# Performance work log

Hardware: AMD Instinct MI355X
Metric: run time of the kernel (lower is better)

Reference implementation:

```python
import jax, jax.numpy as jnp
import numpy as np

# Criteo-like layout
B = 16384          # batch
D = 13             # num dense features
S = 26             # num sparse fields
FEAT = 100000      # one-hot depth per sparse field
K = 64             # FM latent factor dim
TOTAL = D + S * FEAT  # width of the concatenated [dense | one-hot] vector
# column offset of each sparse field's one-hot block inside the stacked vector
OFFSETS = (D + np.arange(S) * FEAT).astype(np.int32)


def setup_inputs() -> dict:
    key = jax.random.key(0)
    k1, k2, k3, k4 = jax.random.split(key, 4)
    dense_inputs = jax.random.normal(k1, (B, D), dtype=jnp.float32)
    sparse_inputs = jax.random.randint(k2, (B, S), 0, FEAT, dtype=jnp.int32)
    # FM parameters over the full stacked feature space [dense | one-hots]
    w = jax.random.normal(k3, (TOTAL, 1), dtype=jnp.float32) * 0.01  # linear weights
    V = jax.random.normal(k4, (TOTAL, K), dtype=jnp.float32) * 0.01  # factor matrix
    b = jnp.zeros((1,), dtype=jnp.float32)                           # bias w0
    return {"dense_inputs": dense_inputs, "sparse_inputs": sparse_inputs,
            "w": w, "V": V, "b": b}


def reference(dense_inputs, sparse_inputs, w, V, b):
    # Fused gather form of: one_hot(sparse) concat dense -> FM.
    # For one-hot columns, x_i is 0/1 so x @ w == gather-sum and x @ V == gather-sum.
    idx = sparse_inputs + jnp.asarray(OFFSETS)[None, :]               # [B, S] global rows
    # ---- first-order (linear) term: x @ w + b ----
    lin = dense_inputs @ w[:D] + jnp.sum(w[idx, 0], axis=1, keepdims=True) + b  # [B, 1]
    # ---- second-order FM term: 0.5 * sum_f [ (x@V)_f^2 - (x^2 @ V^2)_f ] ----
    xv = dense_inputs @ V[:D] + jnp.sum(V[idx], axis=1)               # [B, K]
    x2v2 = (dense_inputs ** 2) @ (V[:D] ** 2) + jnp.sum(V[idx] ** 2, axis=1)  # [B, K]
    inter = 0.5 * jnp.sum(xv * xv - x2v2, axis=1, keepdims=True)      # [B, 1]
    return jax.nn.sigmoid(lin + inter)
```

## Files before the change

kernel.cpp:

```cpp
#include <hip/hip_runtime.h>
#include <math.h>

#define BATCH 16384
#define DNUM  13
#define SNUM  26
#define FEAT  100000
#define KDIM  64
#define RPW   4

__global__ __launch_bounds__(256, 4) void fm_kernel(
    const float*  __restrict__ dense,
    const int*    __restrict__ sparse,
    const float*  __restrict__ w,
    const float4* __restrict__ V4,
    const float*  __restrict__ bias,
    float*        __restrict__ out)
{
    const int wave = (blockIdx.x * blockDim.x + threadIdx.x) >> 6;
    const int lane = threadIdx.x & 63;
    const int g    = lane >> 4;
    const int t    = lane & 15;
    const int row  = wave * RPW + g;
    const int sbase = row * SNUM;

    int idx[SNUM];
    #pragma unroll
    for (int s = 0; s < SNUM; ++s)
        idx[s] = sparse[sbase + s] + DNUM + s * FEAT;

    float lin = w[sparse[sbase + t] + DNUM + t * FEAT];
    if (t < SNUM - 16)
        lin += w[sparse[sbase + t + 16] + DNUM + (t + 16) * FEAT];
    const float* drow = dense + row * DNUM;
    if (t < DNUM)
        lin += drow[t] * w[t];

    float4 xv = make_float4(0.f, 0.f, 0.f, 0.f);
    float  x2 = 0.f;
    #pragma unroll
    for (int s = 0; s < SNUM; ++s) {
        float4 v = V4[idx[s] * 16 + t];
        xv.x += v.x; xv.y += v.y; xv.z += v.z; xv.w += v.w;
        x2   += v.x * v.x + v.y * v.y + v.z * v.z + v.w * v.w;
    }

    #pragma unroll
    for (int d = 0; d < DNUM; ++d) {
        float  xd = drow[d];
        float4 v  = V4[d * 16 + t];
        xv.x += xd * v.x; xv.y += xd * v.y;
        xv.z += xd * v.z; xv.w += xd * v.w;
        x2   += xd * xd * (v.x * v.x + v.y * v.y + v.z * v.z + v.w * v.w);
    }

    float part = 0.5f * (xv.x * xv.x + xv.y * xv.y + xv.z * xv.z + xv.w * xv.w - x2)
               + lin;

    part += __shfl_xor(part, 1);
    part += __shfl_xor(part, 2);
    part += __shfl_xor(part, 4);
    part += __shfl_xor(part, 8);

    if (t == 0) {
        float z = part + bias[0];
        out[row] = 1.0f / (1.0f + expf(-z));
    }
}

extern "C" void kernel_launch(void* const* d_in, const int* in_sizes, int n_in,
                              void* d_out, int out_size, void* d_ws, size_t ws_size,
                              hipStream_t stream) {
    const float*  dense  = (const float*)d_in[0];
    const int*    sparse = (const int*)d_in[1];
    const float*  w      = (const float*)d_in[2];
    const float4* V4     = (const float4*)d_in[3];
    const float*  bias   = (const float*)d_in[4];
    float* out = (float*)d_out;

    const int rows_per_block = (256 / 64) * RPW;
    const int grid = BATCH / rows_per_block;
    fm_kernel<<<grid, 256, 0, stream>>>(dense, sparse, w, V4, bias, out);
}
```

Measured before the change: 732.2 us.

## Split each row across 32 lanes with float2 gathers in batches of seven

```diff
diff --git a/kernel.cpp b/kernel.cpp
--- a/kernel.cpp
+++ b/kernel.cpp
@@ -6,60 +6,70 @@
 #define SNUM  26
 #define FEAT  100000
 #define KDIM  64
-#define RPW   4
+#define RPW   2
+#define GB    7
 
-__global__ __launch_bounds__(256, 4) void fm_kernel(
+__global__ __launch_bounds__(256, 8) void fm_kernel(
     const float*  __restrict__ dense,
     const int*    __restrict__ sparse,
     const float*  __restrict__ w,
-    const float4* __restrict__ V4,
+    const float2* __restrict__ V2,
     const float*  __restrict__ bias,
     float*        __restrict__ out)
 {
     const int wave = (blockIdx.x * blockDim.x + threadIdx.x) >> 6;
     const int lane = threadIdx.x & 63;
-    const int g    = lane >> 4;
-    const int t    = lane & 15;
+    const int g    = lane >> 5;
+    const int t    = lane & 31;
     const int row  = wave * RPW + g;
     const int sbase = row * SNUM;
 
-    int idx[SNUM];
-    #pragma unroll
-    for (int s = 0; s < SNUM; ++s)
-        idx[s] = sparse[sbase + s] + DNUM + s * FEAT;
-
-    float lin = w[sparse[sbase + t] + DNUM + t * FEAT];
-    if (t < SNUM - 16)
-        lin += w[sparse[sbase + t + 16] + DNUM + (t + 16) * FEAT];
+    float lin = 0.f;
+    if (t < SNUM)
+        lin = w[sparse[sbase + t] + DNUM + t * FEAT];
     const float* drow = dense + row * DNUM;
     if (t < DNUM)
         lin += drow[t] * w[t];
 
-    float4 xv = make_float4(0.f, 0.f, 0.f, 0.f);
-    float  x2 = 0.f;
+    float xv0 = 0.f, xv1 = 0.f, x2 = 0.f;
+
+    const char* Vb = (const char*)V2;
     #pragma unroll
-    for (int s = 0; s < SNUM; ++s) {
-        float4 v = V4[idx[s] * 16 + t];
-        xv.x += v.x; xv.y += v.y; xv.z += v.z; xv.w += v.w;
-        x2   += v.x * v.x + v.y * v.y + v.z * v.z + v.w * v.w;
+    for (int b = 0; b < SNUM; b += GB) {
+        const int n = (SNUM - b) < GB ? (SNUM - b) : GB;
+        float2 vb[GB];
+        #pragma unroll
+        for (int j = 0; j < GB; ++j) {
+            if (j < n) {
+                int gi = sparse[sbase + b + j] + DNUM + (b + j) * FEAT;
+                unsigned off = ((unsigned)gi * 32u + (unsigned)t) * 8u;
+                vb[j] = *(const float2*)(Vb + off);
+            }
+        }
+        #pragma unroll
+        for (int j = 0; j < GB; ++j) {
+            if (j < n) {
+                xv0 += vb[j].x; xv1 += vb[j].y;
+                x2  += vb[j].x * vb[j].x + vb[j].y * vb[j].y;
+            }
+        }
     }
 
     #pragma unroll
     for (int d = 0; d < DNUM; ++d) {
         float  xd = drow[d];
-        float4 v  = V4[d * 16 + t];
-        xv.x += xd * v.x; xv.y += xd * v.y;
-        xv.z += xd * v.z; xv.w += xd * v.w;
-        x2   += xd * xd * (v.x * v.x + v.y * v.y + v.z * v.z + v.w * v.w);
+        float2 v  = V2[d * 32 + t];
+        xv0 += xd * v.x; xv1 += xd * v.y;
+        x2  += xd * xd * (v.x * v.x + v.y * v.y);
     }
 
-    float part = 0.5f * (xv.x * xv.x + xv.y * xv.y + xv.z * xv.z + xv.w * xv.w - x2)
-               + lin;
+    float part = 0.5f * (xv0 * xv0 + xv1 * xv1 - x2) + lin;
 
     part += __shfl_xor(part, 1);
     part += __shfl_xor(part, 2);
     part += __shfl_xor(part, 4);
     part += __shfl_xor(part, 8);
+    part += __shfl_xor(part, 16);
 
     if (t == 0) {
         float z = part + bias[0];
@@ -73,11 +83,11 @@
     const float*  dense  = (const float*)d_in[0];
     const int*    sparse = (const int*)d_in[1];
     const float*  w      = (const float*)d_in[2];
-    const float4* V4     = (const float4*)d_in[3];
+    const float2* V2     = (const float2*)d_in[3];
     const float*  bias   = (const float*)d_in[4];
     float* out = (float*)d_out;
 
     const int rows_per_block = (256 / 64) * RPW;
     const int grid = BATCH / rows_per_block;
-    fm_kernel<<<grid, 256, 0, stream>>>(dense, sparse, w, V4, bias, out);
+    fm_kernel<<<grid, 256, 0, stream>>>(dense, sparse, w, V2, bias, out);
 }
```

Result: no change. 736.6 us (+0.6%).
